# Optimization experiments

Measured on AMD Instinct MI355X. Metric: run time of the kernel, lower is better.

Reference implementation:

```python
import jax, jax.numpy as jnp
import numpy as np

N = 100000      # nodes
E = 3200000     # edges (avg degree 32)
G = 2048        # graphs in batch
F_IN = 4        # node feature dim (hardcoded in GCN.__init__)
H = 64          # hidden_dim default


def setup_inputs() -> dict:
    key = jax.random.key(0)
    ks = jax.random.split(key, 9)
    x = jax.random.normal(ks[0], (N, F_IN), dtype=jnp.float32)
    edge_index = jax.random.randint(ks[1], (2, E), 0, N, dtype=jnp.int64)
    batch = jnp.sort(jax.random.randint(ks[2], (N,), 0, G, dtype=jnp.int64))
    # learned params (Glorot-ish scaling)
    W1 = jax.random.normal(ks[3], (F_IN, H), dtype=jnp.float32) * (1.0 / np.sqrt(F_IN))
    b1 = jnp.zeros((H,), jnp.float32)
    W2 = jax.random.normal(ks[4], (H, H), dtype=jnp.float32) * (1.0 / np.sqrt(H))
    b2 = jnp.zeros((H,), jnp.float32)
    Wlin = jax.random.normal(ks[5], (H, 1), dtype=jnp.float32) * (1.0 / np.sqrt(H))
    blin = jnp.zeros((1,), jnp.float32)
    return {"x": x, "edge_index": edge_index, "batch": batch,
            "W1": W1, "b1": b1, "W2": W2, "b2": b2, "Wlin": Wlin, "blin": blin}


def _gcn_conv(x, W, b, src, dst, n):
    # PyG GCNConv: add self-loops, symmetric normalization D^-1/2 A_hat D^-1/2,
    # x' = x @ W, out[dst] += norm * x'[src], plus bias.
    xw = x @ W                                            # [N, H]
    deg = jnp.zeros((n,), xw.dtype).at[dst].add(1.0) + 1.0  # in-degree incl. self-loop
    dinv = jax.lax.rsqrt(deg)                             # deg^{-1/2}
    coef = (dinv[src] * dinv[dst])[:, None]               # [E, 1]
    agg = jax.ops.segment_sum(xw[src] * coef, dst, num_segments=n)  # neighbor msgs
    out = agg + xw * (1.0 / deg)[:, None]                 # self-loop contribution
    return out + b


def _global_mean_pool(x, batch, g):
    sums = jax.ops.segment_sum(x, batch, num_segments=g)
    cnt = jax.ops.segment_sum(jnp.ones((x.shape[0],), x.dtype), batch, num_segments=g)
    return sums / jnp.maximum(cnt, 1.0)[:, None]


def reference(x, edge_index, batch, W1, b1, W2, b2, Wlin, blin):
    src, dst = edge_index[0], edge_index[1]
    h = jax.nn.relu(_gcn_conv(x, W1, b1, src, dst, N))
    h = jax.nn.relu(_gcn_conv(h, W2, b2, src, dst, N))
    p = _global_mean_pool(h, batch, G)                    # [G, H]
    return p @ Wlin + blin                                # [G, 1]
```

## Files before the change

kernel.cpp:

```cpp
#include <hip/hip_runtime.h>
#include <hip/hip_fp16.h>

#define NN 100000
#define NE 3200000
#define NG 2048
#define HD 64
#define BUKSZ 256
#define NBUK 391
#define NB 512
#define CHUNK 6250
#define CAP 9216


typedef __attribute__((ext_vector_type(8))) _Float16 f16x8;
typedef __attribute__((ext_vector_type(4))) float f32x4;
union I4H8 { int4 i4; f16x8 h8; };


__global__ void setup_k(int* __restrict__ bcur, const float* __restrict__ W2,
                        _Float16* __restrict__ W2t) {
    int t = blockIdx.x * blockDim.x + threadIdx.x;
    if (t < HD * HD) {
        int n = t >> 6, k = t & 63;
        W2t[n * HD + k] = (_Float16)W2[k * HD + n];
    }
    int u = t - HD * HD;
    if (u >= 0 && u <= NBUK) bcur[u] = u * CAP;
}


__global__ __launch_bounds__(512) void stageA_k(
        const int* __restrict__ src, const int* __restrict__ dst,
        int* __restrict__ bcur, unsigned int* __restrict__ edges2) {
    __shared__ int hist[NBUK];
    __shared__ int exb[NBUK + 1];
    __shared__ int cur[NBUK];
    __shared__ int obase[NBUK];
    __shared__ int wsum[8];
    __shared__ int wpre[8];
    __shared__ unsigned int svals[CHUNK];
    __shared__ unsigned short sbuk[CHUNK];
    int b = blockIdx.x, t = threadIdx.x;
    int lane = t & 63, wv = t >> 6;
    int base = b * CHUNK;
    for (int i = t; i < NBUK; i += 512) hist[i] = 0;
    __syncthreads();
    for (int i = t; i < CHUNK; i += 512)
        atomicAdd(&hist[dst[base + i] >> 8], 1);
    __syncthreads();
    int v = (t < NBUK) ? hist[t] : 0;
    int x = v;
#pragma unroll
    for (int o = 1; o < 64; o <<= 1) {
        int y = __shfl_up(x, o);
        if (lane >= o) x += y;
    }
    if (lane == 63) wsum[wv] = x;
    __syncthreads();
    if (t == 0) {
        int s = 0;
#pragma unroll
        for (int i = 0; i < 8; ++i) { wpre[i] = s; s += wsum[i]; }
    }
    __syncthreads();
    int excl = x - v + wpre[wv];
    if (t < NBUK) {
        exb[t] = excl;
        cur[t] = excl;
        obase[t] = v ? atomicAdd(&bcur[t], v) : 0;
    }
    if (t == 0) exb[NBUK] = CHUNK;
    __syncthreads();
    for (int i = t; i < CHUNK; i += 512) {
        int d = dst[base + i];
        int s = src[base + i];
        int bk = d >> 8;
        int pos = atomicAdd(&cur[bk], 1);
        svals[pos] = ((unsigned int)(d & 255) << 17) | (unsigned int)s;
        sbuk[pos] = (unsigned short)bk;
    }
    __syncthreads();
    for (int i = t; i < CHUNK; i += 512) {
        int lo = (int)sbuk[i];
        edges2[obase[lo] + (i - exb[lo])] = svals[i];
    }
}


__global__ __launch_bounds__(512) void build1_k(
        const int* __restrict__ bcur, const float4* __restrict__ x,
        unsigned int* __restrict__ edges2, int* __restrict__ row_beg,
        int* __restrict__ row_deg, float* __restrict__ dinv,
        float4* __restrict__ xs) {
    __shared__ unsigned int ebuf[CAP];
    __shared__ int deg[BUKSZ];
    __shared__ int sc[BUKSZ];
    __shared__ int cur[BUKSZ];
    int k = blockIdx.x, t = threadIdx.x;
    int base = k * CAP;
    int len = bcur[k] - base;
    if (t < BUKSZ) deg[t] = 0;
    __syncthreads();
    for (int i = t; i < len; i += 512) {
        unsigned int pv = edges2[base + i];
        ebuf[i] = pv;
        atomicAdd(&deg[pv >> 17], 1);
    }
    __syncthreads();
    int v = 0;
    if (t < BUKSZ) { v = deg[t]; sc[t] = v; }
    __syncthreads();
    for (int o = 1; o < BUKSZ; o <<= 1) {
        int u = 0;
        if (t < BUKSZ && t >= o) u = sc[t - o];
        __syncthreads();
        if (t < BUKSZ && t >= o) sc[t] += u;
        __syncthreads();
    }
    if (t < BUKSZ) {
        int excl = sc[t] - v;
        cur[t] = excl;
        int node = k * BUKSZ + t;
        if (node < NN) {
            row_beg[node] = base + excl;
            row_deg[node] = v;
            float di = rsqrtf((float)v + 1.0f);
            dinv[node] = di;
            float4 xv = x[node];
            xs[node] = make_float4(xv.x * di, xv.y * di, xv.z * di, xv.w * di);
        }
    }
    __syncthreads();
    for (int i = t; i < len; i += 512) {
        unsigned int pv = ebuf[i];
        int pos = atomicAdd(&cur[pv >> 17], 1);
        edges2[base + pos] = pv & 0x1FFFFu;
    }
}


__global__ __launch_bounds__(256) void g1f_k(
        const float4* __restrict__ xs, const unsigned int* __restrict__ csr,
        const int* __restrict__ row_beg, const int* __restrict__ row_deg,
        const float* __restrict__ dinv, const float* __restrict__ W1,
        const float* __restrict__ b1, __half* __restrict__ h1) {
    int wid = (blockIdx.x * blockDim.x + threadIdx.x) >> 6;
    int lane = threadIdx.x & 63;
    if (wid >= NN) return;
    int beg = row_beg[wid], deg = row_deg[wid];
    float sx = 0.f, sy = 0.f, sz = 0.f, sw = 0.f;
    for (int e = beg + lane; e < beg + deg; e += 64) {
        float4 w = xs[csr[e]];
        sx += w.x; sy += w.y; sz += w.z; sw += w.w;
    }
#pragma unroll
    for (int o = 1; o < 64; o <<= 1) {
        sx += __shfl_xor(sx, o);
        sy += __shfl_xor(sy, o);
        sz += __shfl_xor(sz, o);
        sw += __shfl_xor(sw, o);
    }
    float di = dinv[wid];
    float4 self = xs[wid];
    float ax = (sx + self.x) * di;
    float ay = (sy + self.y) * di;
    float az = (sz + self.z) * di;
    float aw = (sw + self.w) * di;
    float v = ax * W1[lane] + ay * W1[64 + lane] + az * W1[128 + lane] + aw * W1[192 + lane] + b1[lane];
    v = fmaxf(v, 0.f) * di;
    h1[(size_t)wid * HD + lane] = __float2half_rn(v);
}


union H8 { int4 i4; __half2 h2[4]; };

__device__ __forceinline__ __half2 shfl_xor_h2(__half2 a, int m) {
    int v = *(int*)&a;
    int s = __shfl_xor(v, m);
    return *(__half2*)&s;
}

__global__ __launch_bounds__(256) void gather2_k(
        const __half* __restrict__ h1, const unsigned int* __restrict__ csr,
        const int* __restrict__ row_beg, const int* __restrict__ row_deg,
        __half* __restrict__ a2h) {
    __shared__ int sidx[4][64];
    int wv = threadIdx.x >> 6;
    int wid = (blockIdx.x * blockDim.x + threadIdx.x) >> 6;
    int lane = threadIdx.x & 63;
    if (wid >= NN) return;
    int half = lane >> 5;
    int g = (lane >> 3) & 3;
    int sub = lane & 7;
    int hg = half * 4 + g;
    int beg = row_beg[wid], deg = row_deg[wid];
    __half2 acc[4];
#pragma unroll
    for (int j = 0; j < 4; ++j) acc[j] = __half2half2(__float2half(0.f));
    int done = 0;
    while (done < deg) {
        int chunk = deg - done;
        if (chunk > 64) chunk = 64;
        if (lane < chunk) sidx[wv][lane] = (int)csr[beg + done + lane];
        int kb = 0;
        for (; kb + 31 < chunk; kb += 32) {
            int e0 = sidx[wv][kb + hg];
            int e1 = sidx[wv][kb + hg + 8];
            int e2 = sidx[wv][kb + hg + 16];
            int e3 = sidx[wv][kb + hg + 24];
            H8 r0, r1, r2, r3;
            r0.i4 = *(const int4*)(h1 + (size_t)e0 * HD + sub * 8);
            r1.i4 = *(const int4*)(h1 + (size_t)e1 * HD + sub * 8);
            r2.i4 = *(const int4*)(h1 + (size_t)e2 * HD + sub * 8);
            r3.i4 = *(const int4*)(h1 + (size_t)e3 * HD + sub * 8);
#pragma unroll
            for (int j = 0; j < 4; ++j) {
                acc[j] = __hadd2(acc[j], __hadd2(__hadd2(r0.h2[j], r1.h2[j]),
                                                 __hadd2(r2.h2[j], r3.h2[j])));
            }
        }
        for (; kb + 7 < chunk; kb += 8) {
            int e0 = sidx[wv][kb + hg];
            H8 r0;
            r0.i4 = *(const int4*)(h1 + (size_t)e0 * HD + sub * 8);
#pragma unroll
            for (int j = 0; j < 4; ++j) acc[j] = __hadd2(acc[j], r0.h2[j]);
        }
        if (kb < chunk) {
            int e = kb + hg;
            if (e < chunk) {
                int e0 = sidx[wv][e];
                H8 r0;
                r0.i4 = *(const int4*)(h1 + (size_t)e0 * HD + sub * 8);
#pragma unroll
                for (int j = 0; j < 4; ++j) acc[j] = __hadd2(acc[j], r0.h2[j]);
            }
        }
        done += chunk;
    }
#pragma unroll
    for (int j = 0; j < 4; ++j) {
        acc[j] = __hadd2(acc[j], shfl_xor_h2(acc[j], 8));
        acc[j] = __hadd2(acc[j], shfl_xor_h2(acc[j], 16));
        acc[j] = __hadd2(acc[j], shfl_xor_h2(acc[j], 32));
    }
    if (half == 0 && g == 0) {
        H8 sv, o;
        sv.i4 = *(const int4*)(h1 + (size_t)wid * HD + sub * 8);
#pragma unroll
        for (int j = 0; j < 4; ++j) o.h2[j] = __hadd2(acc[j], sv.h2[j]);
        ((int4*)a2h)[(size_t)wid * 8 + sub] = o.i4;
    }
}


__global__ __launch_bounds__(256) void c2mfma_k(
        const __half* __restrict__ a2h, const _Float16* __restrict__ W2t,
        const float* __restrict__ b2, const float* __restrict__ dinv,
        const int* __restrict__ batch, float* __restrict__ pool) {
    int tid = threadIdx.x;
    int wave = tid >> 6, lane = tid & 63;
    int base = blockIdx.x * 64 + wave * 16;
    int m = lane & 15, kb = lane >> 4;
    f16x8 bfr[2][4];
#pragma unroll
    for (int kt = 0; kt < 2; ++kt)
#pragma unroll
        for (int nt = 0; nt < 4; ++nt) {
            I4H8 u;
            u.i4 = *(const int4*)(W2t + (nt * 16 + m) * HD + kt * 32 + kb * 8);
            bfr[kt][nt] = u.h8;
        }
    f16x8 afr[2];
    int anode = base + m;
#pragma unroll
    for (int kt = 0; kt < 2; ++kt) {
        I4H8 u;
        if (anode < NN)
            u.i4 = *(const int4*)(a2h + (size_t)anode * HD + kt * 32 + kb * 8);
        else
            u.i4 = make_int4(0, 0, 0, 0);
        afr[kt] = u.h8;
    }
    f32x4 acc[4] = {{0.f, 0.f, 0.f, 0.f}, {0.f, 0.f, 0.f, 0.f},
                    {0.f, 0.f, 0.f, 0.f}, {0.f, 0.f, 0.f, 0.f}};
#pragma unroll
    for (int kt = 0; kt < 2; ++kt)
#pragma unroll
        for (int nt = 0; nt < 4; ++nt)
            acc[nt] = __builtin_amdgcn_mfma_f32_16x16x32_f16(afr[kt], bfr[kt][nt], acc[nt], 0, 0, 0);
    int r0 = base + kb * 4;
    float dv[4];
    int bg[4];
#pragma unroll
    for (int r = 0; r < 4; ++r) {
        int node = r0 + r;
        dv[r] = (node < NN) ? dinv[node] : 0.f;
        bg[r] = (node < NN) ? batch[node] : -1;
    }
#pragma unroll
    for (int nt = 0; nt < 4; ++nt) {
        int n = nt * 16 + m;
        float bv = b2[n];
        int g = -1;
        float accf = 0.f;
#pragma unroll
        for (int r = 0; r < 4; ++r) {
            if (bg[r] < 0) break;
            float v = fmaxf(fmaf(dv[r], acc[nt][r], bv), 0.f);
            if (bg[r] != g) {
                if (g >= 0) atomicAdd(&pool[g * HD + n], accf);
                accf = 0.f; g = bg[r];
            }
            accf += v;
        }
        if (g >= 0) atomicAdd(&pool[g * HD + n], accf);
    }
}

__device__ __forceinline__ int lb_dev(const int* __restrict__ b, int n, int key) {
    int lo = 0, hi = n;
    while (lo < hi) {
        int mid = (lo + hi) >> 1;
        if (b[mid] < key) lo = mid + 1; else hi = mid;
    }
    return lo;
}

__global__ void final_k(const float* __restrict__ pool, const int* __restrict__ batch,
                        const float* __restrict__ Wlin, const float* __restrict__ blin,
                        float* __restrict__ out) {
    int g = blockIdx.x;
    int lane = threadIdx.x;
    int lo = lb_dev(batch, NN, g);
    int hi = lb_dev(batch, NN, g + 1);
    float cnt = (float)(hi - lo);
    float v = pool[g * HD + lane] * Wlin[lane];
#pragma unroll
    for (int off = 32; off > 0; off >>= 1) v += __shfl_down(v, off);
    if (lane == 0) out[g] = v / fmaxf(cnt, 1.0f) + blin[0];
}


extern "C" void kernel_launch(void* const* d_in, const int* in_sizes, int n_in,
                              void* d_out, int out_size, void* d_ws, size_t ws_size,
                              hipStream_t stream) {
    const float* x    = (const float*)d_in[0];
    const int*   ei   = (const int*)d_in[1];
    const int*   bat  = (const int*)d_in[2];
    const float* W1   = (const float*)d_in[3];
    const float* b1   = (const float*)d_in[4];
    const float* W2   = (const float*)d_in[5];
    const float* b2   = (const float*)d_in[6];
    const float* Wlin = (const float*)d_in[7];
    const float* blin = (const float*)d_in[8];
    float* out = (float*)d_out;

    const int* src = ei;
    const int* dst = ei + NE;

    char* ws = (char*)d_ws;
    size_t off = 0;
    auto alloc = [&](size_t bytes) {
        char* p = ws + off;
        off += (bytes + 255) & ~(size_t)255;
        return p;
    };
    int*   bcur    = (int*)  alloc((NBUK + 1) * sizeof(int));
    int*   row_beg = (int*)  alloc(NN * sizeof(int));
    int*   row_deg = (int*)  alloc(NN * sizeof(int));
    float* dinv    = (float*)alloc(NN * sizeof(float));
    unsigned int* edges2 = (unsigned int*)alloc((size_t)NBUK * CAP * sizeof(unsigned int));
    float4* xs     = (float4*)alloc((size_t)NN * sizeof(float4));
    __half* h1     = (__half*)alloc((size_t)NN * HD * sizeof(__half));
    __half* a2h    = (__half*)alloc((size_t)NN * HD * sizeof(__half));
    _Float16* W2t  = (_Float16*)alloc(HD * HD * sizeof(_Float16));
    float* pool    = (float*)alloc((size_t)NG * HD * sizeof(float));
    (void)ws_size; (void)n_in; (void)in_sizes; (void)out_size;

    const int BLK = 256;
    const int gW = (NN * 64 + BLK - 1) / BLK;

    setup_k<<<(HD * HD + NBUK + 1 + 255) / 256, 256, 0, stream>>>(bcur, W2, W2t);
    stageA_k<<<NB, 512, 0, stream>>>(src, dst, bcur, edges2);
    build1_k<<<NBUK, 512, 0, stream>>>(bcur, (const float4*)x, edges2,
                                       row_beg, row_deg, dinv, xs);

    g1f_k<<<gW, BLK, 0, stream>>>(xs, edges2, row_beg, row_deg, dinv, W1, b1, h1);

    gather2_k<<<gW, BLK, 0, stream>>>(h1, edges2, row_beg, row_deg, a2h);

    hipMemsetAsync(pool, 0, (size_t)NG * HD * sizeof(float), stream);
    c2mfma_k<<<(NN + 63) / 64, 256, 0, stream>>>(a2h, W2t, b2, dinv, bat, pool);
    final_k<<<NG, 64, 0, stream>>>(pool, bat, Wlin, blin, out);
}
```

Baseline: 173.2 us.

## Fold pool zeroing into setup kernel, use wave-shuffle scan, widen gather2 blocks

Pool zeroing moves from a separate hipMemsetAsync into setup_k, which removes one launch from the stream. build1_k's shared-memory Hillis-Steele scan with many barriers is replaced by a wave-level shuffle scan plus an 8-entry cross-wave prefix. gather2_k now uses 512-thread blocks with a larger shared index buffer. Together these cut launch overhead and barrier counts, but the larger blocks may change occupancy and scheduling.

Measured after the change: 172.4 us. About the same (-0.5%).

```diff
diff --git a/kernel.cpp b/kernel.cpp
--- a/kernel.cpp
+++ b/kernel.cpp
@@ -18,14 +18,14 @@
 
 
 __global__ void setup_k(int* __restrict__ bcur, const float* __restrict__ W2,
-                        _Float16* __restrict__ W2t) {
+                        _Float16* __restrict__ W2t, float* __restrict__ pool) {
     int t = blockIdx.x * blockDim.x + threadIdx.x;
+    if (t < NG * HD) pool[t] = 0.f;
     if (t < HD * HD) {
         int n = t >> 6, k = t & 63;
         W2t[n * HD + k] = (_Float16)W2[k * HD + n];
     }
-    int u = t - HD * HD;
-    if (u >= 0 && u <= NBUK) bcur[u] = u * CAP;
+    if (t <= NBUK) bcur[t] = t * CAP;
 }
 
 
@@ -94,9 +94,11 @@
         float4* __restrict__ xs) {
     __shared__ unsigned int ebuf[CAP];
     __shared__ int deg[BUKSZ];
-    __shared__ int sc[BUKSZ];
     __shared__ int cur[BUKSZ];
+    __shared__ int wsum[8];
+    __shared__ int wpre[8];
     int k = blockIdx.x, t = threadIdx.x;
+    int lane = t & 63, wv = t >> 6;
     int base = k * CAP;
     int len = bcur[k] - base;
     if (t < BUKSZ) deg[t] = 0;
@@ -107,18 +109,23 @@
         atomicAdd(&deg[pv >> 17], 1);
     }
     __syncthreads();
-    int v = 0;
-    if (t < BUKSZ) { v = deg[t]; sc[t] = v; }
-    __syncthreads();
-    for (int o = 1; o < BUKSZ; o <<= 1) {
-        int u = 0;
-        if (t < BUKSZ && t >= o) u = sc[t - o];
-        __syncthreads();
-        if (t < BUKSZ && t >= o) sc[t] += u;
-        __syncthreads();
-    }
+    int v = (t < BUKSZ) ? deg[t] : 0;
+    int xsc = v;
+#pragma unroll
+    for (int o = 1; o < 64; o <<= 1) {
+        int y = __shfl_up(xsc, o);
+        if (lane >= o) xsc += y;
+    }
+    if (lane == 63) wsum[wv] = xsc;
+    __syncthreads();
+    if (t == 0) {
+        int s = 0;
+#pragma unroll
+        for (int i = 0; i < 8; ++i) { wpre[i] = s; s += wsum[i]; }
+    }
+    __syncthreads();
     if (t < BUKSZ) {
-        int excl = sc[t] - v;
+        int excl = xsc - v + wpre[wv];
         cur[t] = excl;
         int node = k * BUKSZ + t;
         if (node < NN) {
@@ -180,11 +187,11 @@
     return *(__half2*)&s;
 }
 
-__global__ __launch_bounds__(256) void gather2_k(
+__global__ __launch_bounds__(512) void gather2_k(
         const __half* __restrict__ h1, const unsigned int* __restrict__ csr,
         const int* __restrict__ row_beg, const int* __restrict__ row_deg,
         __half* __restrict__ a2h) {
-    __shared__ int sidx[4][64];
+    __shared__ int sidx[8][64];
     int wv = threadIdx.x >> 6;
     int wid = (blockIdx.x * blockDim.x + threadIdx.x) >> 6;
     int lane = threadIdx.x & 63;
@@ -381,16 +388,15 @@
     const int BLK = 256;
     const int gW = (NN * 64 + BLK - 1) / BLK;
 
-    setup_k<<<(HD * HD + NBUK + 1 + 255) / 256, 256, 0, stream>>>(bcur, W2, W2t);
+    setup_k<<<(NG * HD + 255) / 256, 256, 0, stream>>>(bcur, W2, W2t, pool);
     stageA_k<<<NB, 512, 0, stream>>>(src, dst, bcur, edges2);
     build1_k<<<NBUK, 512, 0, stream>>>(bcur, (const float4*)x, edges2,
                                        row_beg, row_deg, dinv, xs);
 
     g1f_k<<<gW, BLK, 0, stream>>>(xs, edges2, row_beg, row_deg, dinv, W1, b1, h1);
 
-    gather2_k<<<gW, BLK, 0, stream>>>(h1, edges2, row_beg, row_deg, a2h);
-
-    hipMemsetAsync(pool, 0, (size_t)NG * HD * sizeof(float), stream);
+    gather2_k<<<(NN * 64 + 511) / 512, 512, 0, stream>>>(h1, edges2, row_beg, row_deg, a2h);
+
     c2mfma_k<<<(NN + 63) / 64, 256, 0, stream>>>(a2h, W2t, b2, dinv, bat, pool);
     final_k<<<NG, 64, 0, stream>>>(pool, bat, Wlin, blin, out);
 }
```
